# Performance work log

Measured on AMD Instinct MI355X. Metric: run time of the kernel, lower is better.

The kernel has to match this reference:

```python
import jax, jax.numpy as jnp
import numpy as np

NUM_CLASSES = 32
TRI = NUM_CLASSES * (NUM_CLASSES - 1) // 2      # 496 class pairs
HID = 32 * TRI                                  # 15872 total hidden
IN = 512
B = 256
RATIO = 0.0

# pair -> (i, j) class indices, in the same enumeration order as the torch idx formula
_I_IDX, _J_IDX = np.triu_indices(NUM_CLASSES, k=1)
_I_IDX = jnp.asarray(_I_IDX)
_J_IDX = jnp.asarray(_J_IDX)


def setup_inputs() -> dict:
    key = jax.random.key(0)
    ks = jax.random.split(key, 7)
    s = 0.02  # small init so activations stay sane
    return {
        "x": jax.random.normal(ks[0], (B, IN), jnp.float32),
        "W1": jax.random.normal(ks[1], (IN, HID), jnp.float32) * s,
        "b1": jax.random.normal(ks[2], (HID,), jnp.float32) * s,
        "W2": jax.random.normal(ks[3], (HID, HID), jnp.float32) * s,
        "b2": jax.random.normal(ks[4], (HID,), jnp.float32) * s,
        "Wout": jax.random.normal(ks[5], (HID, 2 * TRI), jnp.float32) * s,
        "bout": jax.random.normal(ks[6], (2 * TRI,), jnp.float32) * s,
    }


def reference(x, W1, b1, W2, b2, Wout, bout):
    # MLP stack: fc1 + relu, fc2 + relu (num_layers=2), fc_out
    h = jax.nn.relu(x @ W1 + b1)                 # [B, HID]
    h = jax.nn.relu(h @ W2 + b2)                 # [B, HID]
    out = h @ Wout + bout                        # [B, 2*TRI]

    # vote scatter: out[:, 2p], out[:, 2p+1] are the (i, j) logits of pair p
    pair = out.reshape(B, TRI, 2)                # [B, TRI, 2]
    d = pair[..., 0] - pair[..., 1]              # [B, TRI]
    # original condition: d > ratio  OR  -d >= ratio   (always true at ratio=0)
    mask = (d > RATIO) | (-d >= RATIO)
    vi = jnp.where(mask, pair[..., 0], 0.0)      # contribution to class i
    vj = jnp.where(mask, pair[..., 1], 0.0)      # contribution to class j

    votes = jnp.zeros((B, NUM_CLASSES), jnp.float32)
    votes = votes.at[:, _I_IDX].add(vi)
    votes = votes.at[:, _J_IDX].add(vj)
    return votes
```

## Files before the change

### kernel.cpp

```cpp
#include <hip/hip_runtime.h>
#include <hip/hip_bf16.h>

using short8 = __attribute__((ext_vector_type(8))) short;
using f32x16 = __attribute__((ext_vector_type(16))) float;
using us4    = __attribute__((ext_vector_type(4))) unsigned short;

#define NHID 15872

__device__ __forceinline__ unsigned short f2bf(float f) {
  unsigned u = __builtin_bit_cast(unsigned, f);
  u += 0x7fff + ((u >> 16) & 1);
  return (unsigned short)(u >> 16);
}
__device__ __forceinline__ short f2bf_hw(float f) {
  __hip_bfloat16 h = __float2bfloat16(f);
  return __builtin_bit_cast(short, h);
}
__device__ __forceinline__ float bf2f(unsigned short h) {
  return __builtin_bit_cast(float, ((unsigned)h) << 16);
}

__device__ __forceinline__ void gload16(const void* g, void* l) {
  __builtin_amdgcn_global_load_lds(
      (const __attribute__((address_space(1))) unsigned int*)g,
      (__attribute__((address_space(3))) unsigned int*)l, 16, 0, 0);
}

__device__ __forceinline__ size_t pk_idx(int row, int col) {
  return (size_t)(col >> 5) * 8192 + (size_t)((col >> 4) & 1) * 4096 +
         (size_t)(row + 256 * ((col >> 3) & 1)) * 8 + (col & 7);
}

__global__ void cvt_x_pack(const float* __restrict__ x, unsigned short* __restrict__ xpk) {
  int g = blockIdx.x * 256 + threadIdx.x;
  int row = g >> 6, k0 = (g & 63) * 8;
  const float* p = x + (size_t)row * 512 + k0;
  float4 a = *reinterpret_cast<const float4*>(p);
  float4 b = *reinterpret_cast<const float4*>(p + 4);
  us4 o0, o1;
  o0[0] = f2bf(a.x); o0[1] = f2bf(a.y); o0[2] = f2bf(a.z); o0[3] = f2bf(a.w);
  o1[0] = f2bf(b.x); o1[1] = f2bf(b.y); o1[2] = f2bf(b.z); o1[3] = f2bf(b.w);
  unsigned short* d = xpk + pk_idx(row, k0);
  *reinterpret_cast<us4*>(d)     = o0;
  *reinterpret_cast<us4*>(d + 4) = o1;
}


#define WAITV(N) asm volatile("s_waitcnt vmcnt(" #N ")" ::: "memory")

#define STAGE(BUF, T) do { \
    _Pragma("unroll") \
    for (int j_ = 0; j_ < 4; ++j_) \
      gload16(bsrc + ((size_t)(T) * 32 + j_ * 8) * NHID, \
              &Blds[BUF][(j_ * 8 + w) * 256]); \
    { \
      const unsigned short* as_ = apk_src + (size_t)(T) * 8192; \
      gload16(as_,        &Alds[BUF][w * 512]); \
      gload16(as_ + 4096, &Alds[BUF][4096 + w * 512]); \
    } \
  } while (0)

#define COMPUTE(BUF) do { \
    _Pragma("unroll") \
    for (int ks_ = 0; ks_ < 2; ++ks_) { \
      float bf_[8]; \
      _Pragma("unroll") \
      for (int jj_ = 0; jj_ < 8; ++jj_) \
        bf_[jj_] = Blds[BUF][(ks_ * 16 + hi * 8 + jj_) * 256 + w * 32 + l31]; \
      short8 bfr_; \
      _Pragma("unroll") \
      for (int jj_ = 0; jj_ < 8; ++jj_) bfr_[jj_] = f2bf_hw(bf_[jj_]); \
      _Pragma("unroll") \
      for (int rb_ = 0; rb_ < 8; ++rb_) { \
        short8 afr_ = *reinterpret_cast<const short8*>( \
            &Alds[BUF][ks_ * 4096 + (rb_ * 32 + l31 + 256 * hi) * 8]); \
        acc[rb_] = __builtin_amdgcn_mfma_f32_32x32x16_bf16(afr_, bfr_, acc[rb_], 0, 0, 0); \
      } \
    } \
  } while (0)

template<int OUTMODE>
__global__ __launch_bounds__(512, 2)
void gemm_v9(const unsigned short* __restrict__ Apk, int KC,
             const float* __restrict__ B, const float* __restrict__ bias,
             unsigned short* __restrict__ Cf, float* __restrict__ Cp)
{
  __shared__ float Blds[3][32 * 256];
  __shared__ short Alds[3][2 * 4096];

  const int n0   = blockIdx.x * 256;
  const int ks0  = blockIdx.y;
  const int k0   = ks0 * KC;
  const int tid  = threadIdx.x;
  const int w    = tid >> 6;
  const int lane = tid & 63;
  const int l31  = lane & 31;
  const int hi   = lane >> 5;

  f32x16 acc[8] = {};

  const float* bsrc = B + (size_t)(k0 + w) * NHID + n0 + lane * 4;
  const unsigned short* apk_src = Apk + (size_t)(k0 >> 5) * 8192 + tid * 8;

  const int NT = KC >> 5;

  STAGE(0, 0);
  if (NT > 1) STAGE(1, 1);
  if (NT > 2) STAGE(2, 2);
  int cur = 0;
  for (int t = 0; t < NT; ++t) {
    int rem = NT - 1 - t;
    if (rem >= 2)      WAITV(12);
    else if (rem == 1) WAITV(6);
    else               WAITV(0);
    __builtin_amdgcn_sched_barrier(0);
    __builtin_amdgcn_s_barrier();
    COMPUTE(cur);
    __builtin_amdgcn_s_barrier();
    if (t + 3 < NT) STAGE(cur, t + 3);
    cur = (cur == 2) ? 0 : cur + 1;
  }

  const int col = n0 + w * 32 + l31;
  const float bv = (OUTMODE != 1) ? bias[col] : 0.f;
#pragma unroll
  for (int rb = 0; rb < 8; ++rb) {
#pragma unroll
    for (int reg = 0; reg < 16; ++reg) {
      int row = rb * 32 + (reg & 3) + 8 * (reg >> 2) + 4 * hi;
      if (OUTMODE == 0) {
        float v = acc[rb][reg] + bv; v = v > 0.f ? v : 0.f;
        Cf[pk_idx(row, col)] = f2bf(v);
      } else if (OUTMODE == 1) {
        Cp[(size_t)ks0 * 256 * NHID + (size_t)row * NHID + col] = acc[rb][reg];
      } else {
        float v = acc[rb][reg] + bv; v = v > 0.f ? v : 0.f;
        Cf[(size_t)row * NHID + col] = f2bf(v);
      }
    }
  }
}

__global__ void reduce_h2(const float* __restrict__ part, const float* __restrict__ bias,
                          unsigned short* __restrict__ h2, int S) {
  size_t g = ((size_t)blockIdx.x * 256 + threadIdx.x) * 4;
  int c = (int)(g % NHID);
  float4 s = *reinterpret_cast<const float4*>(part + g);
  for (int k = 1; k < S; ++k) {
    float4 p = *reinterpret_cast<const float4*>(part + (size_t)k * 256 * NHID + g);
    s.x += p.x; s.y += p.y; s.z += p.z; s.w += p.w;
  }
  float4 b = *reinterpret_cast<const float4*>(bias + c);
  s.x += b.x; s.y += b.y; s.z += b.z; s.w += b.w;
  us4 o;
  o[0] = f2bf(s.x > 0.f ? s.x : 0.f);
  o[1] = f2bf(s.y > 0.f ? s.y : 0.f);
  o[2] = f2bf(s.z > 0.f ? s.z : 0.f);
  o[3] = f2bf(s.w > 0.f ? s.w : 0.f);
  *reinterpret_cast<us4*>(h2 + g) = o;
}

__global__ void wv_fold(const float* __restrict__ Wout, float* __restrict__ Wv) {
  int g = blockIdx.x * 256 + threadIdx.x;
  int k = g >> 5, c = g & 31;
  const float* row = Wout + (size_t)k * 992;
  float s = 0.f;
#pragma unroll
  for (int o = 0; o < 32; ++o) {
    if (o == c) continue;
    int i = c < o ? c : o;
    int j = c < o ? o : c;
    int p = 31 * i - (i * (i - 1)) / 2 + (j - i - 1);
    s += row[2 * p + (c > o ? 1 : 0)];
  }
  Wv[g] = s;
}

__global__ void votes_partial(const unsigned short* __restrict__ h2,
                              const float* __restrict__ Wv,
                              float* __restrict__ part) {
  int bm = blockIdx.x >> 5;
  int ks = blockIdx.x & 31;
  int r  = bm * 8 + (threadIdx.x >> 5);
  int c  = threadIdx.x & 31;
  const unsigned short* hrow = h2 + (size_t)r * NHID + ks * 496;
  const float* wp = Wv + (size_t)(ks * 496) * 32 + c;
  float s = 0.f;
  for (int k0 = 0; k0 < 496; k0 += 8) {
    short8 hv = *reinterpret_cast<const short8*>(hrow + k0);
#pragma unroll
    for (int j = 0; j < 8; ++j)
      s += bf2f((unsigned short)hv[j]) * wp[(size_t)(k0 + j) * 32];
  }
  part[(size_t)(ks * 256 + r) * 32 + c] = s;
}

__global__ void votes_reduce(const float* __restrict__ part,
                             const float* __restrict__ bout,
                             float* __restrict__ out) {
  int g = blockIdx.x * 256 + threadIdx.x;
  int c = g & 31;
  float s = 0.f;
#pragma unroll
  for (int ks = 0; ks < 32; ++ks) s += part[(size_t)ks * 8192 + g];
  float bv = 0.f;
#pragma unroll
  for (int o = 0; o < 32; ++o) {
    if (o == c) continue;
    int i = c < o ? c : o;
    int j = c < o ? o : c;
    int p = 31 * i - (i * (i - 1)) / 2 + (j - i - 1);
    bv += bout[2 * p + (c > o ? 1 : 0)];
  }
  out[g] = s + bv;
}

extern "C" void kernel_launch(void* const* d_in, const int* in_sizes, int n_in,
                              void* d_out, int out_size, void* d_ws, size_t ws_size,
                              hipStream_t stream) {
  const float* x    = (const float*)d_in[0];
  const float* W1   = (const float*)d_in[1];
  const float* b1   = (const float*)d_in[2];
  const float* W2   = (const float*)d_in[3];
  const float* b2   = (const float*)d_in[4];
  const float* Wout = (const float*)d_in[5];
  const float* bout = (const float*)d_in[6];
  float* out = (float*)d_out;

  char* ws = (char*)d_ws;
  unsigned short* xpk  = (unsigned short*)(ws);
  unsigned short* h1pk = (unsigned short*)(ws + 262144);
  unsigned short* h2   = (unsigned short*)(ws + 8388608);
  float*          Wv   = (float*)(ws + 16515072);
  float*          part = (float*)(ws + 18546688);
  float*         part2 = (float*)(ws + 19595264);

  const size_t PART1 = (size_t)256 * NHID * 4;
  const bool split4 = ws_size >= 19595264ull + 4 * PART1;

  hipLaunchKernelGGL(cvt_x_pack, dim3(64), dim3(256), 0, stream, x, xpk);
  hipLaunchKernelGGL((gemm_v9<0>), dim3(62, 1), dim3(512), 0, stream,
                     xpk, 512, W1, b1, h1pk, (float*)nullptr);
  if (split4) {
    hipLaunchKernelGGL((gemm_v9<1>), dim3(62, 4), dim3(512), 0, stream,
                       h1pk, NHID / 4, W2, (const float*)nullptr,
                       (unsigned short*)nullptr, part2);
    hipLaunchKernelGGL(reduce_h2, dim3(3968), dim3(256), 0, stream, part2, b2, h2, 4);
  } else {
    hipLaunchKernelGGL((gemm_v9<2>), dim3(62, 1), dim3(512), 0, stream,
                       h1pk, NHID, W2, b2, h2, (float*)nullptr);
  }
  hipLaunchKernelGGL(wv_fold,       dim3(1984), dim3(256), 0, stream, Wout, Wv);
  hipLaunchKernelGGL(votes_partial, dim3(1024), dim3(256), 0, stream, h2, Wv, part);
  hipLaunchKernelGGL(votes_reduce,  dim3(32),   dim3(256), 0, stream, part, bout, out);
}
```

Before: 418.2 us.

## Halve GEMM block M-tile, use K16 stages, split-K fc1, XCD-swizzle fc2

Rewrites the GEMM as 256-thread blocks computing a 128x256 tile with 16-deep K stages, doubling the block count so more CUs are busy. The packed activation layout changes to 16-column groups to match. fc1 now also runs split-K with a reduction kernel. fc2 uses a 1D grid swizzled so blocks sharing the same W2 columns land on the same XCD, for better L2 reuse. The cost is that each W2 tile is now read by two M-halves, doubling fp32 weight traffic unless L2 catches the reuse, and fc1 gains an extra partial write and reduction pass.

```diff
diff --git a/kernel.cpp b/kernel.cpp
--- a/kernel.cpp
+++ b/kernel.cpp
@@ -27,7 +27,7 @@
 }
 
 __device__ __forceinline__ size_t pk_idx(int row, int col) {
-  return (size_t)(col >> 5) * 8192 + (size_t)((col >> 4) & 1) * 4096 +
+  return (size_t)(col >> 4) * 4096 +
          (size_t)(row + 256 * ((col >> 3) & 1)) * 8 + (col & 7);
 }
 
@@ -51,45 +51,50 @@
 #define STAGE(BUF, T) do { \
     _Pragma("unroll") \
     for (int j_ = 0; j_ < 4; ++j_) \
-      gload16(bsrc + ((size_t)(T) * 32 + j_ * 8) * NHID, \
-              &Blds[BUF][(j_ * 8 + w) * 256]); \
-    { \
-      const unsigned short* as_ = apk_src + (size_t)(T) * 8192; \
-      gload16(as_,        &Alds[BUF][w * 512]); \
-      gload16(as_ + 4096, &Alds[BUF][4096 + w * 512]); \
+      gload16(bsrc + ((size_t)(T) * 16 + j_) * NHID, &Blds[BUF][(w * 4 + j_) * 256]); \
+    gload16(asrc + (size_t)(T) * 4096, &Alds[BUF][w * 512]); \
+  } while (0)
+
+#define COMPUTE(BUF) do { \
+    short8 bfr_[2]; \
+    _Pragma("unroll") \
+    for (int nb_ = 0; nb_ < 2; ++nb_) { \
+      float tf_[8]; \
+      _Pragma("unroll") \
+      for (int jj_ = 0; jj_ < 8; ++jj_) \
+        tf_[jj_] = Blds[BUF][(hi * 8 + jj_) * 256 + w * 64 + nb_ * 32 + l31]; \
+      _Pragma("unroll") \
+      for (int jj_ = 0; jj_ < 8; ++jj_) bfr_[nb_][jj_] = f2bf_hw(tf_[jj_]); \
+    } \
+    _Pragma("unroll") \
+    for (int rb_ = 0; rb_ < 4; ++rb_) { \
+      short8 afr_ = *reinterpret_cast<const short8*>( \
+          &Alds[BUF][hi * 1024 + (rb_ * 32 + l31) * 8]); \
+      acc[rb_ * 2 + 0] = __builtin_amdgcn_mfma_f32_32x32x16_bf16(afr_, bfr_[0], acc[rb_ * 2 + 0], 0, 0, 0); \
+      acc[rb_ * 2 + 1] = __builtin_amdgcn_mfma_f32_32x32x16_bf16(afr_, bfr_[1], acc[rb_ * 2 + 1], 0, 0, 0); \
     } \
   } while (0)
 
-#define COMPUTE(BUF) do { \
-    _Pragma("unroll") \
-    for (int ks_ = 0; ks_ < 2; ++ks_) { \
-      float bf_[8]; \
-      _Pragma("unroll") \
-      for (int jj_ = 0; jj_ < 8; ++jj_) \
-        bf_[jj_] = Blds[BUF][(ks_ * 16 + hi * 8 + jj_) * 256 + w * 32 + l31]; \
-      short8 bfr_; \
-      _Pragma("unroll") \
-      for (int jj_ = 0; jj_ < 8; ++jj_) bfr_[jj_] = f2bf_hw(bf_[jj_]); \
-      _Pragma("unroll") \
-      for (int rb_ = 0; rb_ < 8; ++rb_) { \
-        short8 afr_ = *reinterpret_cast<const short8*>( \
-            &Alds[BUF][ks_ * 4096 + (rb_ * 32 + l31 + 256 * hi) * 8]); \
-        acc[rb_] = __builtin_amdgcn_mfma_f32_32x32x16_bf16(afr_, bfr_, acc[rb_], 0, 0, 0); \
-      } \
-    } \
-  } while (0)
-
-template<int OUTMODE>
-__global__ __launch_bounds__(512, 2)
-void gemm_v9(const unsigned short* __restrict__ Apk, int KC,
-             const float* __restrict__ B, const float* __restrict__ bias,
-             unsigned short* __restrict__ Cf, float* __restrict__ Cp)
+template<int OUTMODE, bool SWZ>
+__global__ __launch_bounds__(256, 2)
+void gemm_v10(const unsigned short* __restrict__ Apk, int KC,
+              const float* __restrict__ B, const float* __restrict__ bias,
+              unsigned short* __restrict__ Cf, float* __restrict__ Cp)
 {
-  __shared__ float Blds[3][32 * 256];
-  __shared__ short Alds[3][2 * 4096];
-
-  const int n0   = blockIdx.x * 256;
-  const int ks0  = blockIdx.y;
+  __shared__ float Blds[3][16 * 256];
+  __shared__ short Alds[3][2048];
+
+  int nidx, ks0, mh;
+  if (SWZ) {
+    int b = blockIdx.x;
+    int g = b >> 4, r = b & 15, xcd = r & 7;
+    mh   = r >> 3;
+    ks0  = xcd >> 1;
+    nidx = g * 2 + (xcd & 1);
+  } else {
+    mh = blockIdx.x & 1; nidx = blockIdx.x >> 1; ks0 = blockIdx.y;
+  }
+  const int n0   = nidx * 256;
   const int k0   = ks0 * KC;
   const int tid  = threadIdx.x;
   const int w    = tid >> 6;
@@ -99,20 +104,18 @@
 
   f32x16 acc[8] = {};
 
-  const float* bsrc = B + (size_t)(k0 + w) * NHID + n0 + lane * 4;
-  const unsigned short* apk_src = Apk + (size_t)(k0 >> 5) * 8192 + tid * 8;
-
-  const int NT = KC >> 5;
-
-  STAGE(0, 0);
-  if (NT > 1) STAGE(1, 1);
-  if (NT > 2) STAGE(2, 2);
+  const float* bsrc = B + (size_t)(k0 + w * 4) * NHID + n0 + lane * 4;
+  const unsigned short* asrc = Apk + ((size_t)k0 >> 4) * 4096 +
+      (w >> 1) * 2048 + mh * 1024 + (w & 1) * 512 + lane * 8;
+
+  const int NT = KC >> 4;
+
+  STAGE(0, 0); STAGE(1, 1); STAGE(2, 2);
   int cur = 0;
   for (int t = 0; t < NT; ++t) {
-    int rem = NT - 1 - t;
-    if (rem >= 2)      WAITV(12);
-    else if (rem == 1) WAITV(6);
-    else               WAITV(0);
+    if (t + 2 < NT)      WAITV(10);
+    else if (t + 1 < NT) WAITV(5);
+    else                 WAITV(0);
     __builtin_amdgcn_sched_barrier(0);
     __builtin_amdgcn_s_barrier();
     COMPUTE(cur);
@@ -121,33 +124,40 @@
     cur = (cur == 2) ? 0 : cur + 1;
   }
 
-  const int col = n0 + w * 32 + l31;
-  const float bv = (OUTMODE != 1) ? bias[col] : 0.f;
-#pragma unroll
-  for (int rb = 0; rb < 8; ++rb) {
-#pragma unroll
-    for (int reg = 0; reg < 16; ++reg) {
-      int row = rb * 32 + (reg & 3) + 8 * (reg >> 2) + 4 * hi;
-      if (OUTMODE == 0) {
-        float v = acc[rb][reg] + bv; v = v > 0.f ? v : 0.f;
-        Cf[pk_idx(row, col)] = f2bf(v);
-      } else if (OUTMODE == 1) {
-        Cp[(size_t)ks0 * 256 * NHID + (size_t)row * NHID + col] = acc[rb][reg];
-      } else {
-        float v = acc[rb][reg] + bv; v = v > 0.f ? v : 0.f;
-        Cf[(size_t)row * NHID + col] = f2bf(v);
+#pragma unroll
+  for (int rb = 0; rb < 4; ++rb) {
+#pragma unroll
+    for (int nb = 0; nb < 2; ++nb) {
+      int col = n0 + w * 64 + nb * 32 + l31;
+      float bv = (OUTMODE != 1) ? bias[col] : 0.f;
+#pragma unroll
+      for (int reg = 0; reg < 16; ++reg) {
+        int row = mh * 128 + rb * 32 + (reg & 3) + 8 * (reg >> 2) + 4 * hi;
+        float v = acc[rb * 2 + nb][reg];
+        if (OUTMODE == 0) {
+          v += bv; v = v > 0.f ? v : 0.f;
+          Cf[pk_idx(row, col)] = f2bf(v);
+        } else if (OUTMODE == 1) {
+          Cp[(size_t)ks0 * 256 * NHID + (size_t)row * NHID + col] = v;
+        } else {
+          v += bv; v = v > 0.f ? v : 0.f;
+          Cf[(size_t)row * NHID + col] = f2bf(v);
+        }
       }
     }
   }
 }
 
-__global__ void reduce_h2(const float* __restrict__ part, const float* __restrict__ bias,
-                          unsigned short* __restrict__ h2, int S) {
-  size_t g = ((size_t)blockIdx.x * 256 + threadIdx.x) * 4;
-  int c = (int)(g % NHID);
-  float4 s = *reinterpret_cast<const float4*>(part + g);
+template<bool PACK>
+__global__ void reduce_h(const float* __restrict__ part, const float* __restrict__ bias,
+                         unsigned short* __restrict__ out, int S) {
+  int g4 = blockIdx.x * 256 + threadIdx.x;
+  int row = g4 / 3968;
+  int c   = (g4 - row * 3968) * 4;
+  size_t off = (size_t)row * NHID + c;
+  float4 s = *reinterpret_cast<const float4*>(part + off);
   for (int k = 1; k < S; ++k) {
-    float4 p = *reinterpret_cast<const float4*>(part + (size_t)k * 256 * NHID + g);
+    float4 p = *reinterpret_cast<const float4*>(part + (size_t)k * 256 * NHID + off);
     s.x += p.x; s.y += p.y; s.z += p.z; s.w += p.w;
   }
   float4 b = *reinterpret_cast<const float4*>(bias + c);
@@ -157,7 +167,8 @@
   o[1] = f2bf(s.y > 0.f ? s.y : 0.f);
   o[2] = f2bf(s.z > 0.f ? s.z : 0.f);
   o[3] = f2bf(s.w > 0.f ? s.w : 0.f);
-  *reinterpret_cast<us4*>(h2 + g) = o;
+  if (PACK) *reinterpret_cast<us4*>(out + pk_idx(row, c)) = o;
+  else      *reinterpret_cast<us4*>(out + off) = o;
 }
 
 __global__ void wv_fold(const float* __restrict__ Wout, float* __restrict__ Wv) {
@@ -236,18 +247,24 @@
   float*         part2 = (float*)(ws + 19595264);
 
   const size_t PART1 = (size_t)256 * NHID * 4;
-  const bool split4 = ws_size >= 19595264ull + 4 * PART1;
+  const bool split = ws_size >= 19595264ull + 4 * PART1;
 
   hipLaunchKernelGGL(cvt_x_pack, dim3(64), dim3(256), 0, stream, x, xpk);
-  hipLaunchKernelGGL((gemm_v9<0>), dim3(62, 1), dim3(512), 0, stream,
-                     xpk, 512, W1, b1, h1pk, (float*)nullptr);
-  if (split4) {
-    hipLaunchKernelGGL((gemm_v9<1>), dim3(62, 4), dim3(512), 0, stream,
-                       h1pk, NHID / 4, W2, (const float*)nullptr,
+  if (split) {
+    hipLaunchKernelGGL((gemm_v10<1, false>), dim3(124, 2), dim3(256), 0, stream,
+                       xpk, 256, W1, (const float*)nullptr,
                        (unsigned short*)nullptr, part2);
-    hipLaunchKernelGGL(reduce_h2, dim3(3968), dim3(256), 0, stream, part2, b2, h2, 4);
+    hipLaunchKernelGGL((reduce_h<true>), dim3(3968), dim3(256), 0, stream,
+                       part2, b1, h1pk, 2);
+    hipLaunchKernelGGL((gemm_v10<1, true>), dim3(496), dim3(256), 0, stream,
+                       h1pk, 3968, W2, (const float*)nullptr,
+                       (unsigned short*)nullptr, part2);
+    hipLaunchKernelGGL((reduce_h<false>), dim3(3968), dim3(256), 0, stream,
+                       part2, b2, h2, 4);
   } else {
-    hipLaunchKernelGGL((gemm_v9<2>), dim3(62, 1), dim3(512), 0, stream,
+    hipLaunchKernelGGL((gemm_v10<0, false>), dim3(124, 1), dim3(256), 0, stream,
+                       xpk, 512, W1, b1, h1pk, (float*)nullptr);
+    hipLaunchKernelGGL((gemm_v10<2, false>), dim3(124, 1), dim3(256), 0, stream,
                        h1pk, NHID, W2, b2, h2, (float*)nullptr);
   }
   hipLaunchKernelGGL(wv_fold,       dim3(1984), dim3(256), 0, stream, Wout, Wv);
```

Result: slower. 455.9 us (+9.0%).
